# Kernel optimization log

Hardware: AMD Instinct MI355X
Metric: run time of the kernel (lower is better)

The kernel has to match this reference:

```python
import jax, jax.numpy as jnp
import numpy as np
import math

B, S, D, H, DF, L = 8, 1024, 1024, 16, 4096, 2
DK = D // H

def cosine_pe(seq_len, d_model):
    pos = jnp.arange(seq_len, dtype=jnp.float32)[:, None]
    div = jnp.exp(jnp.arange(0, d_model, 2, dtype=jnp.float32) * (-math.log(10000.0) / d_model))
    ang = pos * div[None, :]  # [S, D/2]
    # interleave sin (even cols) and cos (odd cols)
    return jnp.stack([jnp.sin(ang), jnp.cos(ang)], axis=-1).reshape(seq_len, d_model)

def layernorm(x, g, b, eps=1e-5):
    m = jnp.mean(x, axis=-1, keepdims=True)
    v = jnp.mean((x - m) ** 2, axis=-1, keepdims=True)
    return (x - m) / jnp.sqrt(v + eps) * g + b

def setup_inputs() -> dict:
    key = jax.random.key(0)
    ks = jax.random.split(key, 8)
    w = 0.03  # ~xavier scale for d_model=1024
    return {
        "q_embed_data": jax.random.normal(ks[0], (B, S, D), dtype=jnp.float32),
        "qa_embed_data": jax.random.normal(ks[1], (B, S, D), dtype=jnp.float32),
        "Wk": jax.random.normal(ks[2], (L, D, D), dtype=jnp.float32) * w,
        "bk": jnp.zeros((L, D), jnp.float32),
        "Wv": jax.random.normal(ks[3], (L, D, D), dtype=jnp.float32) * w,
        "bv": jnp.zeros((L, D), jnp.float32),
        "Wo": jax.random.normal(ks[4], (L, D, D), dtype=jnp.float32) * w,
        "bo": jnp.zeros((L, D), jnp.float32),
        "ln1_g": jnp.ones((L, D), jnp.float32),
        "ln1_b": jnp.zeros((L, D), jnp.float32),
        "W1": jax.random.normal(ks[5], (L, DF, D), dtype=jnp.float32) * w,
        "b1": jnp.zeros((L, DF), jnp.float32),
        "W2": jax.random.normal(ks[6], (L, D, DF), dtype=jnp.float32) * w,
        "b2": jnp.zeros((L, D), jnp.float32),
        "ln2_g": jnp.ones((L, D), jnp.float32),
        "ln2_b": jnp.zeros((L, D), jnp.float32),
    }

def reference(q_embed_data, qa_embed_data, Wk, bk, Wv, bv, Wo, bo, ln1_g, ln1_b, W1, b1, W2, b2, ln2_g, ln2_b):
    b, s, d = q_embed_data.shape
    pe = cosine_pe(s, d)
    x = q_embed_data + pe[None]   # query/key stream, updated per block
    y = qa_embed_data + pe[None]  # value stream, fixed across blocks
    idx = jnp.arange(s)
    allow = idx[None, :] < idx[:, None]  # strict causal: only past (j < i)
    n_blocks = Wk.shape[0]
    for l in range(n_blocks):
        # kq_same=True: q and k share k_linear
        q = (x @ Wk[l].T + bk[l]).reshape(b, s, H, DK).transpose(0, 2, 1, 3)
        k = q  # same input and same projection
        v = (y @ Wv[l].T + bv[l]).reshape(b, s, H, DK).transpose(0, 2, 1, 3)
        scores = jnp.einsum('bhid,bhjd->bhij', q, k) / math.sqrt(DK)
        scores = jnp.where(allow[None, None], scores, jnp.float32(-1e32))
        p = jax.nn.softmax(scores, axis=-1)
        p = p.at[:, :, 0, :].set(0.0)  # zero_pad first query row
        attn = jnp.einsum('bhij,bhjd->bhid', p, v).transpose(0, 2, 1, 3).reshape(b, s, d)
        attn = attn @ Wo[l].T + bo[l]
        x = layernorm(x + attn, ln1_g[l], ln1_b[l])
        ff = jax.nn.relu(x @ W1[l].T + b1[l]) @ W2[l].T + b2[l]
        x = layernorm(x + ff, ln2_g[l], ln2_b[l])
    return x
```

## Files before the change

### kernel.cpp

```cpp
#include <hip/hip_runtime.h>

using bf16   = __bf16;
using bf16x4 = __attribute__((ext_vector_type(4))) __bf16;
using bf16x8 = __attribute__((ext_vector_type(8))) __bf16;
using f32x4  = __attribute__((ext_vector_type(4))) float;

#define GLDS16(g, l)                                                            \
  __builtin_amdgcn_global_load_lds(                                             \
      (__attribute__((address_space(1))) void*)(g),                             \
      (__attribute__((address_space(3))) void*)(l), 16, 0, 0)

#define MFMA16(a, b, c) __builtin_amdgcn_mfma_f32_16x16x32_bf16(a, b, c, 0, 0, 0)

__device__ __forceinline__ int SW(int r, int s) {
  return r * 64 + (((s ^ (r & 7) ^ ((r >> 3) & 7)) & 7) << 3);
}

__device__ __forceinline__ float b2f(unsigned short u) {
  return (float)__builtin_bit_cast(bf16, u);
}

__device__ __forceinline__ bf16x8 scale8th(bf16x8 v) {
  bf16x8 r;
#pragma unroll
  for (int i = 0; i < 8; ++i) r[i] = (bf16)((float)v[i] * 0.125f);
  return r;
}

__global__ __launch_bounds__(256)
void init_pe(const float4* __restrict__ qd, const float4* __restrict__ qa,
             ushort4* __restrict__ xbf, ushort4* __restrict__ ybf) {
  const int n4 = 8 * 1024 * 1024 / 4;
  for (int i = blockIdx.x * 256 + threadIdx.x; i < n4; i += gridDim.x * 256) {
    int d4 = (i & 255) * 4;
    int ss = (i >> 8) & 1023;
    const float c = -0.0089944730195177f;
    float a0 = (float)ss * __expf((float)d4 * c);
    float a1 = (float)ss * __expf((float)(d4 + 2) * c);
    float p0 = sinf(a0), p1 = cosf(a0), p2 = sinf(a1), p3 = cosf(a1);
    float4 q4 = qd[i], y4 = qa[i];
    ushort4 xb, yb;
    xb.x = __builtin_bit_cast(unsigned short, (bf16)(q4.x + p0));
    xb.y = __builtin_bit_cast(unsigned short, (bf16)(q4.y + p1));
    xb.z = __builtin_bit_cast(unsigned short, (bf16)(q4.z + p2));
    xb.w = __builtin_bit_cast(unsigned short, (bf16)(q4.w + p3));
    yb.x = __builtin_bit_cast(unsigned short, (bf16)(y4.x + p0));
    yb.y = __builtin_bit_cast(unsigned short, (bf16)(y4.y + p1));
    yb.z = __builtin_bit_cast(unsigned short, (bf16)(y4.z + p2));
    yb.w = __builtin_bit_cast(unsigned short, (bf16)(y4.w + p3));
    xbf[i] = xb; ybf[i] = yb;
  }
}

__global__ __launch_bounds__(256)
void cvt5(const float4* __restrict__ s0, const float4* __restrict__ s1,
          const float4* __restrict__ s2, const float4* __restrict__ s3,
          const float4* __restrict__ s4,
          ushort4* __restrict__ dDD, ushort4* __restrict__ dDF,
          int n4dd, int n4df) {
  const int z = blockIdx.z;
  const float4* s = (z == 0) ? s0 : (z == 1) ? s1 : (z == 2) ? s2 : (z == 3) ? s3 : s4;
  ushort4* dd = (z < 3) ? dDD + (size_t)z * n4dd : dDF + (size_t)(z - 3) * n4df;
  const int n4 = (z < 3) ? n4dd : n4df;
  for (int i = blockIdx.x * 256 + threadIdx.x; i < n4; i += gridDim.x * 256) {
    float4 v = s[i];
    ushort4 o;
    o.x = __builtin_bit_cast(unsigned short, (bf16)v.x);
    o.y = __builtin_bit_cast(unsigned short, (bf16)v.y);
    o.z = __builtin_bit_cast(unsigned short, (bf16)v.z);
    o.w = __builtin_bit_cast(unsigned short, (bf16)v.w);
    dd[i] = o;
  }
}

template <int EPI, int MODE>
__global__ __launch_bounds__(256, 4)
void gemm_s(const bf16* __restrict__ A0, const bf16* __restrict__ W0,
            const float* __restrict__ b0, void* __restrict__ C0,
            const bf16* __restrict__ A1, const bf16* __restrict__ W1,
            const float* __restrict__ b1, void* __restrict__ C1,
            const int N, const int K) {
  __shared__ bf16 L[2][128 * 64];

  const int tid = threadIdx.x;
  const int wave = tid >> 6, lane = tid & 63;
  const int wm = wave >> 1, wn = wave & 1;
  const int cl = lane & 15, hk = lane >> 4;

  const int gx = gridDim.x;
  int flat = blockIdx.y * gx + blockIdx.x;
  flat = (flat & 7) * ((gx * gridDim.y) >> 3) + (flat >> 3);
  const int bcol = flat % gx, brow = flat / gx;
  const int z = (MODE == 0) ? 0 : blockIdx.z;

  const bf16* A = (MODE == 1 && z) ? A1 : A0;
  const bf16* W = (MODE == 1 && z) ? W1 : W0;
  const float* bias = (MODE == 1 && z) ? b1 : b0;
  void* C = (MODE == 1 && z) ? C1 : C0;

  const bf16* Ablk = A + (size_t)brow * 128 * K;
  const bf16* Wblk = W + (size_t)bcol * 128 * K;

  const int strow8 = lane >> 3;
  const int sl8 = (lane & 7) ^ (lane >> 3);

#define STAGE(kt)                                                               \
  do {                                                                          \
    _Pragma("unroll") for (int i_ = 0; i_ < 4; ++i_) {                          \
      int r0_ = i_ * 32 + wave * 8;                                             \
      GLDS16(Ablk + (size_t)(r0_ + strow8) * K + (size_t)(kt) * 64 + sl8 * 8,   \
             &L[0][r0_ * 64]);                                                  \
      GLDS16(Wblk + (size_t)(r0_ + strow8) * K + (size_t)(kt) * 64 + sl8 * 8,   \
             &L[1][r0_ * 64]);                                                  \
    }                                                                           \
  } while (0)

#define RD(reg, r_, kk_) \
  (*(const bf16x8*)&L[reg][(r_) * 64 + ((((kk_) * 4 + hk) ^ (cl & 7)) * 8)])

  f32x4 acc[4][4] = {};
  const int NT = K >> 6;

  for (int t = 0; t < NT; ++t) {
    STAGE(t);
    __syncthreads();
#pragma unroll
    for (int kk = 0; kk < 2; ++kk) {
      bf16x8 a4[4], b4[4];
#pragma unroll
      for (int m = 0; m < 4; ++m) a4[m] = RD(0, wm * 64 + m * 16 + cl, kk);
#pragma unroll
      for (int n = 0; n < 4; ++n) b4[n] = RD(1, wn * 64 + n * 16 + cl, kk);
      __builtin_amdgcn_s_setprio(1);
#pragma unroll
      for (int m = 0; m < 4; ++m)
#pragma unroll
        for (int n = 0; n < 4; ++n)
          acc[m][n] = MFMA16(a4[m], b4[n], acc[m][n]);
      __builtin_amdgcn_s_setprio(0);
    }
    __syncthreads();
  }
#undef STAGE
#undef RD

  float bv[4];
#pragma unroll
  for (int n = 0; n < 4; ++n)
    bv[n] = bias[bcol * 128 + wn * 64 + n * 16 + cl];

  const int crow0 = brow * 128 + wm * 64;
  const int ccol0 = bcol * 128 + wn * 64;
  char* esmem = (char*)(&L[0][0]) + wave * 4608;

  if (MODE == 1 && z == 1) {
    bf16* ep = (bf16*)esmem;
    const int h_ = ccol0 >> 6;
#pragma unroll
    for (int mp = 0; mp < 2; ++mp) {
#pragma unroll
      for (int mb = 0; mb < 2; ++mb) {
        int m = mp * 2 + mb;
#pragma unroll
        for (int n = 0; n < 4; ++n) {
          bf16x4 w4;
#pragma unroll
          for (int j = 0; j < 4; ++j) w4[j] = (bf16)(acc[m][n][j] + bv[n]);
          *(bf16x4*)&ep[(n * 16 + cl) * 36 + mb * 16 + hk * 4] = w4;
        }
      }
      asm volatile("s_waitcnt lgkmcnt(0)" ::: "memory");
      __builtin_amdgcn_sched_barrier(0);
      {
        const int t0 = crow0 + mp * 32;
        const int b_ = t0 >> 10, s_ = t0 & 1023;
        bf16* dst = (bf16*)C + ((size_t)(b_ * 16 + h_) * 64 + lane) * 1024 + s_;
        const bf16* src = &ep[lane * 36];
#pragma unroll
        for (int i = 0; i < 4; ++i)
          *(bf16x8*)&dst[i * 8] = *(const bf16x8*)&src[i * 8];
      }
      asm volatile("s_waitcnt lgkmcnt(0)" ::: "memory");
      __builtin_amdgcn_sched_barrier(0);
    }
  } else {
#pragma unroll
    for (int m = 0; m < 4; ++m) {
      bf16* ep = (bf16*)esmem;
#pragma unroll
      for (int n = 0; n < 4; ++n)
#pragma unroll
        for (int j = 0; j < 4; ++j) {
          float val = acc[m][n][j] + bv[n];
          if (EPI == 1) val = fmaxf(val, 0.f);
          ep[(hk * 4 + j) * 64 + n * 16 + cl] = (bf16)val;
        }
      asm volatile("s_waitcnt lgkmcnt(0)" ::: "memory");
      __builtin_amdgcn_sched_barrier(0);
#pragma unroll
      for (int i = 0; i < 2; ++i) {
        bf16x8 vv = ((const bf16x8*)ep)[lane + i * 64];
        const int row = crow0 + m * 16 + 8 * i + (lane >> 3);
        *(bf16x8*)((bf16*)C + (size_t)row * N + ccol0 + (lane & 7) * 8) = vv;
      }
      asm volatile("s_waitcnt lgkmcnt(0)" ::: "memory");
      __builtin_amdgcn_sched_barrier(0);
    }
  }
}

template <int EPI, int K>
__global__ __launch_bounds__(512, 2)
void gemm8(const bf16* __restrict__ A, const bf16* __restrict__ W,
           const float* __restrict__ bias, bf16* __restrict__ C, const int N) {
  extern __shared__ bf16 lds[];
  constexpr int NT = K >> 6;

  const int tid = threadIdx.x;
  const int wave = tid >> 6, lane = tid & 63;
  const int wm = wave >> 2, wn = wave & 3;
  const int cl = lane & 15, hk = lane >> 4;
  const int c7 = cl & 7;
  const int sl8 = (lane & 7) ^ (lane >> 3);

  const int gx = gridDim.x;
  int flat = blockIdx.y * gx + blockIdx.x;
  flat = (flat & 7) * ((gx * gridDim.y) >> 3) + (flat >> 3);
  const int bcol = flat % gx, brow = flat / gx;

  const size_t srow = (size_t)(wave * 8 + (lane >> 3)) * K + sl8 * 8;
  const bf16* pA = A + (size_t)brow * 256 * K + srow;
  const bf16* pW = W + (size_t)bcol * 256 * K + srow;
  bf16* ldsw = lds + wave * 512;

  int bA_[2][2], bB_[2][2];
#pragma unroll
  for (int b_ = 0; b_ < 2; ++b_)
#pragma unroll
    for (int kk = 0; kk < 2; ++kk) {
      const int slot = ((kk * 4 + hk) ^ c7) * 16;
      bA_[b_][kk] = b_ * 65536 + (wm * 128 + cl) * 128 + slot;
      bB_[b_][kk] = b_ * 65536 + 32768 + (wn * 64 + cl) * 128 + slot;
    }

#define STG2(src, coff, roff, dstoff)                                          \
  do {                                                                         \
    _Pragma("unroll") for (int i_ = 0; i_ < 2; ++i_)                           \
      GLDS16((src) + (coff) + (size_t)((roff) + i_ * 64) * K,                  \
             ldsw + (dstoff) + i_ * 4096);                                     \
  } while (0)

#define LDA8(bf_, kk_, mh_, m_) \
  (*(const bf16x8*)((const char*)lds + bA_[bf_][kk_] + (mh_)*8192 + (m_)*2048))
#define LDB8(bf_, kk_, nh_, n_) \
  (*(const bf16x8*)((const char*)lds + bB_[bf_][kk_] + (nh_)*4096 + (n_)*2048))

#define BAR8 asm volatile("s_barrier" ::: "memory")
#define LGKM0 do { asm volatile("s_waitcnt lgkmcnt(0)" ::: "memory"); \
                   __builtin_amdgcn_sched_barrier(0); } while (0)

  STG2(pA, 0, 0, 0);
  STG2(pW, 0, 0, 16384);
  STG2(pA, 0, 128, 8192);
  STG2(pW, 0, 128, 16384 + 8192);
  STG2(pW, 64, 0, 32768 + 16384);
  STG2(pA, 64, 0, 32768);
  asm volatile("s_waitcnt vmcnt(4)" ::: "memory");
  BAR8;

  f32x4 acc[2][2][4][2] = {};
  bf16x8 af[2][4], b0f[2][2], b1f[2][2];

#pragma unroll 2
  for (int t = 0; t < NT; ++t) {
    const int bf_ = t & 1, nb_ = bf_ ^ 1;
    const int co = t * 64;

#pragma unroll
    for (int kk = 0; kk < 2; ++kk) {
#pragma unroll
      for (int m_ = 0; m_ < 4; ++m_) af[kk][m_] = LDA8(bf_, kk, 0, m_);
#pragma unroll
      for (int n_ = 0; n_ < 2; ++n_) b0f[kk][n_] = LDB8(bf_, kk, 0, n_);
    }
    if (t + 1 < NT) {
      STG2(pA, co + 64, 128, nb_ * 32768 + 8192);
      STG2(pW, co + 64, 128, nb_ * 32768 + 16384 + 8192);
    }
    asm volatile("s_waitcnt lgkmcnt(8)" ::: "memory");
    BAR8;
    LGKM0;
    __builtin_amdgcn_s_setprio(1);
#pragma unroll
    for (int kk = 0; kk < 2; ++kk)
#pragma unroll
      for (int m_ = 0; m_ < 4; ++m_)
#pragma unroll
        for (int n_ = 0; n_ < 2; ++n_)
          acc[0][0][m_][n_] = MFMA16(af[kk][m_], b0f[kk][n_], acc[0][0][m_][n_]);
    __builtin_amdgcn_s_setprio(0);
    BAR8;

#pragma unroll
    for (int kk = 0; kk < 2; ++kk)
#pragma unroll
      for (int n_ = 0; n_ < 2; ++n_) b1f[kk][n_] = LDB8(bf_, kk, 1, n_);
    BAR8;
    LGKM0;
    __builtin_amdgcn_s_setprio(1);
#pragma unroll
    for (int kk = 0; kk < 2; ++kk)
#pragma unroll
      for (int m_ = 0; m_ < 4; ++m_)
#pragma unroll
        for (int n_ = 0; n_ < 2; ++n_)
          acc[0][1][m_][n_] = MFMA16(af[kk][m_], b1f[kk][n_], acc[0][1][m_][n_]);
    __builtin_amdgcn_s_setprio(0);
    BAR8;

#pragma unroll
    for (int kk = 0; kk < 2; ++kk)
#pragma unroll
      for (int m_ = 0; m_ < 4; ++m_) af[kk][m_] = LDA8(bf_, kk, 1, m_);
    if (t + 2 < NT) STG2(pW, co + 128, 0, bf_ * 32768 + 16384);
    BAR8;
    LGKM0;
    __builtin_amdgcn_s_setprio(1);
#pragma unroll
    for (int kk = 0; kk < 2; ++kk)
#pragma unroll
      for (int m_ = 0; m_ < 4; ++m_)
#pragma unroll
        for (int n_ = 0; n_ < 2; ++n_)
          acc[1][0][m_][n_] = MFMA16(af[kk][m_], b0f[kk][n_], acc[1][0][m_][n_]);
    __builtin_amdgcn_s_setprio(0);
    BAR8;

    if (t + 2 < NT) STG2(pA, co + 128, 0, bf_ * 32768);
    BAR8;
    __builtin_amdgcn_s_setprio(1);
#pragma unroll
    for (int kk = 0; kk < 2; ++kk)
#pragma unroll
      for (int m_ = 0; m_ < 4; ++m_)
#pragma unroll
        for (int n_ = 0; n_ < 2; ++n_)
          acc[1][1][m_][n_] = MFMA16(af[kk][m_], b1f[kk][n_], acc[1][1][m_][n_]);
    __builtin_amdgcn_s_setprio(0);
    if (t + 2 < NT) {
      asm volatile("s_waitcnt vmcnt(4)" ::: "memory");
    } else {
      asm volatile("s_waitcnt vmcnt(0)" ::: "memory");
    }
    BAR8;
  }
#undef STG2
#undef LDA8
#undef LDB8
#undef BAR8
#undef LGKM0

  __syncthreads();

  float bv[2][2];
#pragma unroll
  for (int nh = 0; nh < 2; ++nh)
#pragma unroll
    for (int n_ = 0; n_ < 2; ++n_)
      bv[nh][n_] = bias[bcol * 256 + wn * 64 + nh * 32 + n_ * 16 + cl];

  const int crow0 = brow * 256 + wm * 128;
  const int ccol0 = bcol * 256 + wn * 64;
  bf16* ep = lds + wave * 2304;

#pragma unroll
  for (int mh = 0; mh < 2; ++mh)
#pragma unroll
    for (int m_ = 0; m_ < 4; ++m_) {
#pragma unroll
      for (int nh = 0; nh < 2; ++nh)
#pragma unroll
        for (int n_ = 0; n_ < 2; ++n_)
#pragma unroll
          for (int j = 0; j < 4; ++j) {
            float val = acc[mh][nh][m_][n_][j] + bv[nh][n_];
            if (EPI == 1) val = fmaxf(val, 0.f);
            ep[(hk * 4 + j) * 64 + nh * 32 + n_ * 16 + cl] = (bf16)val;
          }
      asm volatile("s_waitcnt lgkmcnt(0)" ::: "memory");
      __builtin_amdgcn_sched_barrier(0);
#pragma unroll
      for (int i = 0; i < 2; ++i) {
        bf16x8 vv = ((const bf16x8*)ep)[lane + i * 64];
        const int row = crow0 + mh * 64 + m_ * 16 + 8 * i + (lane >> 3);
        *(bf16x8*)(C + (size_t)row * N + ccol0 + (lane & 7) * 8) = vv;
      }
      asm volatile("s_waitcnt lgkmcnt(0)" ::: "memory");
      __builtin_amdgcn_sched_barrier(0);
    }
}

#define SOFTMAX_PV(sc_, diag_, mreg, lreg, oacc)                                 \
  do {                                                                           \
    if (diag_) {                                                                 \
      _Pragma("unroll") for (int c = 0; c < 4; ++c)                              \
        _Pragma("unroll") for (int j = 0; j < 4; ++j)                            \
          if (c * 16 + hk * 4 + j >= wave * 16 + cl) sc_[c][j] = -1e30f;         \
    }                                                                            \
    float rl_[4];                                                                \
    _Pragma("unroll") for (int c = 0; c < 4; ++c)                                \
      rl_[c] = fmaxf(fmaxf(sc_[c][0], sc_[c][1]), fmaxf(sc_[c][2], sc_[c][3]));  \
    float rloc_ = fmaxf(fmaxf(rl_[0], rl_[1]), fmaxf(rl_[2], rl_[3]));           \
    if (!__all(rloc_ <= mreg)) {                                                 \
      float rmx_ = fmaxf(rloc_, __shfl_xor(rloc_, 16));                          \
      rmx_ = fmaxf(rmx_, __shfl_xor(rmx_, 32));                                  \
      float mn_ = fmaxf(mreg, rmx_);                                             \
      float sca_ = __expf(mreg - mn_);                                           \
      mreg = mn_;                                                                \
      lreg *= sca_;                                                              \
      float scr_[4];                                                             \
      _Pragma("unroll") for (int j = 0; j < 4; ++j)                              \
        scr_[j] = __shfl(sca_, hk * 4 + j);                                      \
      _Pragma("unroll") for (int c = 0; c < 4; ++c)                              \
        _Pragma("unroll") for (int j = 0; j < 4; ++j) oacc[c][j] *= scr_[j];     \
    }                                                                            \
    float ps_ = 0.f;                                                             \
    if (diag_) {                                                                 \
      _Pragma("unroll") for (int c = 0; c < 4; ++c) {                            \
        bf16x4 pk_;                                                              \
        _Pragma("unroll") for (int j = 0; j < 4; ++j) {                          \
          float e_ = (sc_[c][j] < -1e29f) ? 0.f : __expf(sc_[c][j] - mreg);      \
          ps_ += e_;                                                             \
          pk_[j] = (bf16)e_;                                                     \
        }                                                                        \
        *(bf16x4*)&Pw[SW(cl, c * 2 + (hk >> 1)) + (hk & 1) * 4] = pk_;           \
      }                                                                          \
    } else {                                                                     \
      _Pragma("unroll") for (int c = 0; c < 4; ++c) {                            \
        bf16x4 pk_;                                                              \
        _Pragma("unroll") for (int j = 0; j < 4; ++j) {                          \
          float e_ = __expf(sc_[c][j] - mreg);                                   \
          ps_ += e_;                                                             \
          pk_[j] = (bf16)e_;                                                     \
        }                                                                        \
        *(bf16x4*)&Pw[SW(cl, c * 2 + (hk >> 1)) + (hk & 1) * 4] = pk_;           \
      }                                                                          \
    }                                                                            \
    lreg += ps_;                  \
    const bf16x8 pa0_ = *(const bf16x8*)&Pw[SW(cl, hk)];                         \
    const bf16x8 pa1_ = *(const bf16x8*)&Pw[SW(cl, 4 + hk)];                     \
    __builtin_amdgcn_s_setprio(1);                                               \
    _Pragma("unroll") for (int c = 0; c < 4; ++c) {                              \
      const bf16x8 vf0_ = *(const bf16x8*)&Vb[SW(c * 16 + cl, hk)];              \
      const bf16x8 vf1_ = *(const bf16x8*)&Vb[SW(c * 16 + cl, 4 + hk)];          \
      oacc[c] = MFMA16(pa0_, vf0_, oacc[c]);                                     \
      oacc[c] = MFMA16(pa1_, vf1_, oacc[c]);                                     \
    }                                                                            \
    __builtin_amdgcn_s_setprio(0);                                               \
  } while (0)

__global__ __launch_bounds__(256, 2)
void attn_kernel(const bf16* __restrict__ q, const bf16* __restrict__ vT,
                 bf16* __restrict__ out) {
  const int S = 1024, D = 1024;
  const int f = blockIdx.y * 8 + blockIdx.x;
  const int g = f >> 3, xcd = f & 7;
  const int qa = g >> 4;
  const int bh = xcd * 16 + (g & 15);
  const int qb = 15 - qa;
  const int b = bh >> 4, h = bh & 15;
  const int tid = threadIdx.x, wave = tid >> 6, lane = tid & 63;

  __shared__ bf16 Ks[2][4096];
  __shared__ bf16 Vt[2][4096];
  __shared__ bf16 Ps[4][1024];

  const bf16* qp = q + (size_t)b * S * D + h * 64;
  const bf16* vp = vT + (size_t)(b * 16 + h) * 64 * 1024;

  const int cl = lane & 15;
  const int hk = lane >> 4;
  const int r0 = hk * 4;
  const int k8 = hk * 8;

  const int ksrow = lane >> 3;
  const int ksslot = (lane & 7) ^ (lane >> 3);

  const int rA = qa * 64 + wave * 16 + cl;
  const int rB = qb * 64 + wave * 16 + cl;
  const bf16x8 qA0 = scale8th(*(const bf16x8*)(qp + (size_t)rA * D + k8));
  const bf16x8 qA1 = scale8th(*(const bf16x8*)(qp + (size_t)rA * D + 32 + k8));
  const bf16x8 qB0 = scale8th(*(const bf16x8*)(qp + (size_t)rB * D + k8));
  const bf16x8 qB1 = scale8th(*(const bf16x8*)(qp + (size_t)rB * D + 32 + k8));

  f32x4 oA[4] = {}, oB[4] = {};
  float mA_ = -1e30f, lA_ = 0.f, mB_ = -1e30f, lB_ = 0.f;

  bf16* Pw = Ps[wave];
  int buf = 0;

#define STAGE_KV(dst_ks, dst_vt, jt_)                                            \
  do {                                                                           \
    _Pragma("unroll") for (int j = 0; j < 2; ++j) {                              \
      int ch = wave * 2 + j;                                                     \
      GLDS16(qp + (size_t)((jt_) * 64 + ch * 8 + ksrow) * D +                    \
                 ((ksslot ^ (ch & 7)) * 8),                                      \
             (dst_ks) + ch * 512);                                               \
      GLDS16(vp + (size_t)(ch * 8 + ksrow) * 1024 + (jt_) * 64 +                 \
                 ((ksslot ^ (ch & 7)) * 8),                                      \
             (dst_vt) + ch * 512);                                               \
    }                                                                            \
  } while (0)

  STAGE_KV(&Ks[0][0], &Vt[0][0], 0);
  __syncthreads();

  for (int jt = 0; jt <= qb; ++jt) {
    const int nxt = buf ^ 1;
    if (jt < qb) STAGE_KV(&Ks[nxt][0], &Vt[nxt][0], jt + 1);

    {
      const bf16* Kb = Ks[buf];
      const bf16* Vb = Vt[buf];
      const bool doA = (jt <= qa);
      const bool diagB = (jt == qb), diagA = (jt == qa);

      f32x4 scB[4], scA[4];
      __builtin_amdgcn_s_setprio(1);
#pragma unroll
      for (int c = 0; c < 4; ++c) {
        int r_ = c * 16 + cl;
        const bf16x8 kf0 = *(const bf16x8*)&Kb[SW(r_, hk)];
        const bf16x8 kf1 = *(const bf16x8*)&Kb[SW(r_, 4 + hk)];
        f32x4 zB = {};
        zB = MFMA16(kf0, qB0, zB);
        zB = MFMA16(kf1, qB1, zB);
        scB[c] = zB;
        if (doA) {
          f32x4 zA = {};
          zA = MFMA16(kf0, qA0, zA);
          zA = MFMA16(kf1, qA1, zA);
          scA[c] = zA;
        }
      }
      __builtin_amdgcn_s_setprio(0);

      SOFTMAX_PV(scB, diagB, mB_, lB_, oB);
      if (doA) SOFTMAX_PV(scA, diagA, mA_, lA_, oA);
    }
    __syncthreads();
    buf = nxt;
  }
#undef STAGE_KV

  lA_ += __shfl_xor(lA_, 16);
  lA_ += __shfl_xor(lA_, 32);
  lB_ += __shfl_xor(lB_, 16);
  lB_ += __shfl_xor(lB_, 32);

  bf16* ob = out + (size_t)b * S * D + h * 64;
  const float invA = (lA_ > 0.f) ? 1.f / lA_ : 0.f;
  const float invB = (lB_ > 0.f) ? 1.f / lB_ : 0.f;
#pragma unroll
  for (int j = 0; j < 4; ++j) {
    const float iA = __shfl(invA, hk * 4 + j);
    const float iB = __shfl(invB, hk * 4 + j);
    {
      int row = qa * 64 + wave * 16 + r0 + j;
#pragma unroll
      for (int c = 0; c < 4; ++c)
        ob[(size_t)row * D + c * 16 + cl] = (bf16)(oA[c][j] * iA);
    }
    {
      int row = qb * 64 + wave * 16 + r0 + j;
#pragma unroll
      for (int c = 0; c < 4; ++c)
        ob[(size_t)row * D + c * 16 + cl] = (bf16)(oB[c][j] * iB);
    }
  }
}

__global__ __launch_bounds__(256)
void add_ln(const ushort4* __restrict__ xin, const ushort4* __restrict__ y1b,
            const float* __restrict__ g, const float* __restrict__ bt,
            ushort4* __restrict__ xbf, float4* __restrict__ xout) {
  const int row = blockIdx.x;
  const int tid = threadIdx.x;
  const int wave = tid >> 6, lane = tid & 63;
  const size_t base4 = (size_t)row * 256 + tid;
  ushort4 a4 = xin[base4];
  ushort4 c4 = y1b[base4];
  float v0 = b2f(a4.x) + b2f(c4.x), v1 = b2f(a4.y) + b2f(c4.y);
  float v2 = b2f(a4.z) + b2f(c4.z), v3 = b2f(a4.w) + b2f(c4.w);

  float s = v0 + v1 + v2 + v3;
#pragma unroll
  for (int off = 32; off; off >>= 1) s += __shfl_xor(s, off);
  __shared__ float red1[4], red2[4];
  if (lane == 0) red1[wave] = s;
  __syncthreads();
  float mean = (red1[0] + red1[1] + red1[2] + red1[3]) * (1.f / 1024.f);

  float d0 = v0 - mean, d1 = v1 - mean, d2 = v2 - mean, d3 = v3 - mean;
  float vs = d0 * d0 + d1 * d1 + d2 * d2 + d3 * d3;
#pragma unroll
  for (int off = 32; off; off >>= 1) vs += __shfl_xor(vs, off);
  if (lane == 0) red2[wave] = vs;
  __syncthreads();
  float var = (red2[0] + red2[1] + red2[2] + red2[3]) * (1.f / 1024.f);
  float rstd = rsqrtf(var + 1e-5f);

  const int col = tid * 4;
  float4 gg = *(const float4*)(g + col);
  float4 bb = *(const float4*)(bt + col);
  float o0 = d0 * rstd * gg.x + bb.x;
  float o1 = d1 * rstd * gg.y + bb.y;
  float o2 = d2 * rstd * gg.z + bb.z;
  float o3 = d3 * rstd * gg.w + bb.w;
  if (xout) {
    float4 oo; oo.x = o0; oo.y = o1; oo.z = o2; oo.w = o3;
    xout[base4] = oo;
  } else {
    ushort4 ob;
    ob.x = __builtin_bit_cast(unsigned short, (bf16)o0);
    ob.y = __builtin_bit_cast(unsigned short, (bf16)o1);
    ob.z = __builtin_bit_cast(unsigned short, (bf16)o2);
    ob.w = __builtin_bit_cast(unsigned short, (bf16)o3);
    xbf[base4] = ob;
  }
}

extern "C" void kernel_launch(void* const* d_in, const int* in_sizes, int n_in,
                              void* d_out, int out_size, void* d_ws, size_t ws_size,
                              hipStream_t stream) {
  const float* qd  = (const float*)d_in[0];
  const float* qa  = (const float*)d_in[1];
  const float* Wk  = (const float*)d_in[2];
  const float* bk  = (const float*)d_in[3];
  const float* Wv  = (const float*)d_in[4];
  const float* bv  = (const float*)d_in[5];
  const float* Wo  = (const float*)d_in[6];
  const float* bo  = (const float*)d_in[7];
  const float* l1g = (const float*)d_in[8];
  const float* l1b = (const float*)d_in[9];
  const float* W1  = (const float*)d_in[10];
  const float* b1  = (const float*)d_in[11];
  const float* W2  = (const float*)d_in[12];
  const float* b2  = (const float*)d_in[13];
  const float* l2g = (const float*)d_in[14];
  const float* l2b = (const float*)d_in[15];

  const size_t DD = 1024 * 1024, DFD = 4096 * 1024, T = 8192;
  bf16* wkb = (bf16*)d_ws;
  bf16* wvb = wkb + 2 * DD;
  bf16* wob = wvb + 2 * DD;
  bf16* w1b = wob + 2 * DD;
  bf16* w2b = w1b + 2 * DFD;
  bf16* regA = w2b + 2 * DFD;
  bf16* qbf = regA;
  bf16* vbf = regA + 8388608;
  bf16* abf = regA + 16777216;
  bf16* ff1 = regA;
  bf16* xbf = regA + 33554432;
  bf16* ybf = xbf + 8388608;
  bf16* g1b = ybf + 8388608;

  static bool gemm8_attr = false;
  if (!gemm8_attr) {
    (void)hipFuncSetAttribute(reinterpret_cast<const void*>(&gemm8<1, 1024>),
                              hipFuncAttributeMaxDynamicSharedMemorySize, 131072);
    gemm8_attr = true;
  }

  init_pe<<<2048, 256, 0, stream>>>((const float4*)qd, (const float4*)qa,
                                    (ushort4*)xbf, (ushort4*)ybf);
  cvt5<<<dim3(1024, 1, 5), 256, 0, stream>>>(
      (const float4*)Wk, (const float4*)Wv, (const float4*)Wo,
      (const float4*)W1, (const float4*)W2,
      (ushort4*)wkb, (ushort4*)w1b, (int)(2 * DD / 4), (int)(2 * DFD / 4));

  for (int l = 0; l < 2; ++l) {
    gemm_s<0, 1><<<dim3(8, 64, 2), 256, 0, stream>>>(
        xbf, wkb + l * DD, bk + l * 1024, qbf,
        ybf, wvb + l * DD, bv + l * 1024, vbf, 1024, 1024);
    attn_kernel<<<dim3(8, 128), 256, 0, stream>>>(qbf, vbf, abf);
    gemm_s<0, 0><<<dim3(8, 64), 256, 0, stream>>>(
        abf, wob + l * DD, bo + l * 1024, g1b, nullptr, nullptr, nullptr, nullptr, 1024, 1024);
    add_ln<<<T, 256, 0, stream>>>((const ushort4*)xbf, (const ushort4*)g1b,
                                  l1g + l * 1024, l1b + l * 1024,
                                  (ushort4*)xbf, nullptr);
    gemm8<1, 1024><<<dim3(16, 32), 512, 131072, stream>>>(
        xbf, w1b + l * DFD, b1 + l * 4096, ff1, 4096);
    gemm_s<0, 0><<<dim3(8, 64), 256, 0, stream>>>(
        ff1, w2b + l * DFD, b2 + l * 1024, g1b, nullptr, nullptr, nullptr, nullptr, 1024, 4096);
    const bool last = (l == 1);
    add_ln<<<T, 256, 0, stream>>>((const ushort4*)xbf, (const ushort4*)g1b,
                                  l2g + l * 1024, l2b + l * 1024,
                                  (ushort4*)xbf, last ? (float4*)d_out : nullptr);
  }
  (void)in_sizes; (void)n_in; (void)out_size; (void)ws_size;
}
```

Before: 602.9 us.

## Restructure GEMM main loop into ping-pong pipeline with cross-tile A-fragment prefetch

Rewrites the 256x256 GEMM K-loop as a macro-unrolled pipeline with double A fragment registers (afP/afQ). The next tile's A fragments are prefetched during the last MFMA quadrant, and the global-to-LDS staging is reordered so B halves are issued together and A halves later. Waitcnt thresholds are tuned to overlap LDS reads with MFMA work. It aims to cut barrier stalls and LDS latency exposure, at the cost of more registers and a requirement that NT be even and at least 4.

```diff
diff --git a/kernel.cpp b/kernel.cpp
--- a/kernel.cpp
+++ b/kernel.cpp
@@ -215,6 +215,7 @@
            const float* __restrict__ bias, bf16* __restrict__ C, const int N) {
   extern __shared__ bf16 lds[];
   constexpr int NT = K >> 6;
+  static_assert(NT >= 4 && (NT & 1) == 0, "NT even, >=4");
 
   const int tid = threadIdx.x;
   const int wave = tid >> 6, lane = tid & 63;
@@ -256,109 +257,105 @@
   (*(const bf16x8*)((const char*)lds + bB_[bf_][kk_] + (nh_)*4096 + (n_)*2048))
 
 #define BAR8 asm volatile("s_barrier" ::: "memory")
-#define LGKM0 do { asm volatile("s_waitcnt lgkmcnt(0)" ::: "memory"); \
-                   __builtin_amdgcn_sched_barrier(0); } while (0)
+#define SB0 __builtin_amdgcn_sched_barrier(0)
+
+  f32x4 acc[2][2][4][2] = {};
+  bf16x8 afP[2][4], afQ[2][4], b0[2][2], b1[2][2];
 
   STG2(pA, 0, 0, 0);
+  STG2(pA, 0, 128, 8192);
   STG2(pW, 0, 0, 16384);
-  STG2(pA, 0, 128, 8192);
   STG2(pW, 0, 128, 16384 + 8192);
-  STG2(pW, 64, 0, 32768 + 16384);
   STG2(pA, 64, 0, 32768);
+  STG2(pA, 64, 128, 32768 + 8192);
   asm volatile("s_waitcnt vmcnt(4)" ::: "memory");
   BAR8;
-
-  f32x4 acc[2][2][4][2] = {};
-  bf16x8 af[2][4], b0f[2][2], b1f[2][2];
-
-#pragma unroll 2
-  for (int t = 0; t < NT; ++t) {
-    const int bf_ = t & 1, nb_ = bf_ ^ 1;
-    const int co = t * 64;
-
-#pragma unroll
-    for (int kk = 0; kk < 2; ++kk) {
-#pragma unroll
-      for (int m_ = 0; m_ < 4; ++m_) af[kk][m_] = LDA8(bf_, kk, 0, m_);
-#pragma unroll
-      for (int n_ = 0; n_ < 2; ++n_) b0f[kk][n_] = LDB8(bf_, kk, 0, n_);
-    }
-    if (t + 1 < NT) {
-      STG2(pA, co + 64, 128, nb_ * 32768 + 8192);
-      STG2(pW, co + 64, 128, nb_ * 32768 + 16384 + 8192);
-    }
-    asm volatile("s_waitcnt lgkmcnt(8)" ::: "memory");
-    BAR8;
-    LGKM0;
-    __builtin_amdgcn_s_setprio(1);
-#pragma unroll
-    for (int kk = 0; kk < 2; ++kk)
-#pragma unroll
-      for (int m_ = 0; m_ < 4; ++m_)
-#pragma unroll
-        for (int n_ = 0; n_ < 2; ++n_)
-          acc[0][0][m_][n_] = MFMA16(af[kk][m_], b0f[kk][n_], acc[0][0][m_][n_]);
-    __builtin_amdgcn_s_setprio(0);
-    BAR8;
-
-#pragma unroll
-    for (int kk = 0; kk < 2; ++kk)
-#pragma unroll
-      for (int n_ = 0; n_ < 2; ++n_) b1f[kk][n_] = LDB8(bf_, kk, 1, n_);
-    BAR8;
-    LGKM0;
-    __builtin_amdgcn_s_setprio(1);
-#pragma unroll
-    for (int kk = 0; kk < 2; ++kk)
-#pragma unroll
-      for (int m_ = 0; m_ < 4; ++m_)
-#pragma unroll
-        for (int n_ = 0; n_ < 2; ++n_)
-          acc[0][1][m_][n_] = MFMA16(af[kk][m_], b1f[kk][n_], acc[0][1][m_][n_]);
-    __builtin_amdgcn_s_setprio(0);
-    BAR8;
-
-#pragma unroll
-    for (int kk = 0; kk < 2; ++kk)
-#pragma unroll
-      for (int m_ = 0; m_ < 4; ++m_) af[kk][m_] = LDA8(bf_, kk, 1, m_);
-    if (t + 2 < NT) STG2(pW, co + 128, 0, bf_ * 32768 + 16384);
-    BAR8;
-    LGKM0;
-    __builtin_amdgcn_s_setprio(1);
-#pragma unroll
-    for (int kk = 0; kk < 2; ++kk)
-#pragma unroll
-      for (int m_ = 0; m_ < 4; ++m_)
-#pragma unroll
-        for (int n_ = 0; n_ < 2; ++n_)
-          acc[1][0][m_][n_] = MFMA16(af[kk][m_], b0f[kk][n_], acc[1][0][m_][n_]);
-    __builtin_amdgcn_s_setprio(0);
-    BAR8;
-
-    if (t + 2 < NT) STG2(pA, co + 128, 0, bf_ * 32768);
-    BAR8;
-    __builtin_amdgcn_s_setprio(1);
-#pragma unroll
-    for (int kk = 0; kk < 2; ++kk)
-#pragma unroll
-      for (int m_ = 0; m_ < 4; ++m_)
-#pragma unroll
-        for (int n_ = 0; n_ < 2; ++n_)
-          acc[1][1][m_][n_] = MFMA16(af[kk][m_], b1f[kk][n_], acc[1][1][m_][n_]);
-    __builtin_amdgcn_s_setprio(0);
-    if (t + 2 < NT) {
-      asm volatile("s_waitcnt vmcnt(4)" ::: "memory");
-    } else {
-      asm volatile("s_waitcnt vmcnt(0)" ::: "memory");
-    }
-    BAR8;
-  }
+#pragma unroll
+  for (int kk = 0; kk < 2; ++kk)
+#pragma unroll
+    for (int m_ = 0; m_ < 4; ++m_) afP[kk][m_] = LDA8(0, kk, 0, m_);
+
+#define MF_Q(mh, nh, AF, BF)                                                   \
+  do {                                                                         \
+    __builtin_amdgcn_s_setprio(1);                                             \
+    _Pragma("unroll") for (int kk = 0; kk < 2; ++kk)                           \
+      _Pragma("unroll") for (int m_ = 0; m_ < 4; ++m_)                         \
+        _Pragma("unroll") for (int n_ = 0; n_ < 2; ++n_)                       \
+          acc[mh][nh][m_][n_] =                                                \
+              MFMA16(AF[kk][m_], BF[kk][n_], acc[mh][nh][m_][n_]);             \
+    __builtin_amdgcn_s_setprio(0);                                             \
+  } while (0)
+
+#define TILE8(bf_, nb_, co, DO_BH, DO_AH, VM4, VM0, DO_PF)                     \
+  do {                                                                         \
+                                                                 \
+    if (DO_BH) {                                                               \
+      STG2(pW, (co) + 64, 0, (nb_)*32768 + 16384);                             \
+      STG2(pW, (co) + 64, 128, (nb_)*32768 + 16384 + 8192);                    \
+    }                                                                          \
+    BAR8;                                                                      \
+    _Pragma("unroll") for (int kk = 0; kk < 2; ++kk)                           \
+      _Pragma("unroll") for (int n_ = 0; n_ < 2; ++n_)                         \
+        b0[kk][n_] = LDB8(bf_, kk, 0, n_);                                     \
+    _Pragma("unroll") for (int kk = 0; kk < 2; ++kk)                           \
+      _Pragma("unroll") for (int n_ = 0; n_ < 2; ++n_)                         \
+        b1[kk][n_] = LDB8(bf_, kk, 1, n_);                                     \
+    asm volatile("s_waitcnt lgkmcnt(4)" ::: "memory");                         \
+    SB0;                                                                       \
+    MF_Q(0, 0, afP, b0);                                                       \
+    BAR8;                                                                      \
+                                                                 \
+    _Pragma("unroll") for (int kk = 0; kk < 2; ++kk)                           \
+      _Pragma("unroll") for (int m_ = 0; m_ < 4; ++m_)                         \
+        afQ[kk][m_] = LDA8(bf_, kk, 1, m_);                                    \
+    asm volatile("s_waitcnt lgkmcnt(8)" ::: "memory");                         \
+    SB0;                                                                       \
+    MF_Q(0, 1, afP, b1);                                                       \
+    BAR8;                                                                      \
+                                                                 \
+    _Pragma("unroll") for (int kk = 0; kk < 2; ++kk)                           \
+      _Pragma("unroll") for (int n_ = 0; n_ < 2; ++n_)                         \
+        b0[kk][n_] = LDB8(bf_, kk, 0, n_);                                     \
+    asm volatile("s_waitcnt lgkmcnt(4)" ::: "memory");                         \
+    SB0;                                                                       \
+    MF_Q(1, 1, afQ, b1);                                                       \
+    BAR8;                                                                      \
+                                                                 \
+    if (DO_AH) {                                                               \
+      STG2(pA, (co) + 128, 0, (bf_)*32768);                                    \
+      STG2(pA, (co) + 128, 128, (bf_)*32768 + 8192);                           \
+    }                                                                          \
+    if (VM4) asm volatile("s_waitcnt vmcnt(4)" ::: "memory");                  \
+    else if (VM0) asm volatile("s_waitcnt vmcnt(0)" ::: "memory");             \
+    BAR8;                                                                      \
+    if (DO_PF) {                                                               \
+      _Pragma("unroll") for (int kk = 0; kk < 2; ++kk)                         \
+        _Pragma("unroll") for (int m_ = 0; m_ < 4; ++m_)                       \
+          afP[kk][m_] = LDA8(nb_, kk, 0, m_);                                  \
+      asm volatile("s_waitcnt lgkmcnt(8)" ::: "memory");                       \
+    } else {                                                                   \
+      asm volatile("s_waitcnt lgkmcnt(0)" ::: "memory");                       \
+    }                                                                          \
+    SB0;                                                                       \
+    MF_Q(1, 0, afQ, b0);                                                       \
+    BAR8;                                                                      \
+  } while (0)
+
+  for (int tp = 0; tp < (NT - 2) / 2; ++tp) {
+    const int co = tp * 128;
+    TILE8(0, 1, co, 1, 1, 1, 0, 1);
+    TILE8(1, 0, co + 64, 1, 1, 1, 0, 1);
+  }
+  TILE8(0, 1, (NT - 2) * 64, 1, 0, 0, 1, 1);
+  TILE8(1, 0, (NT - 1) * 64, 0, 0, 0, 0, 0);
+
+#undef TILE8
+#undef MF_Q
 #undef STG2
 #undef LDA8
 #undef LDB8
 #undef BAR8
-#undef LGKM0
+#undef SB0
 
   __syncthreads();
 
```

After: 607.3 us. About the same (+0.7%).
